# Kernel optimization log

Measured on AMD Instinct MI355X. Metric: run time of the kernel, lower is better.

Reference implementation:

```python
import jax, jax.numpy as jnp
import numpy as np

N, E = 100000, 1600000
IN_DIM, H, D = 128, 4, 32
ALPHA = 0.2  # leaky relu negative slope


def setup_inputs() -> dict:
    key = jax.random.key(0)
    k1, k2, k3, k4, k5, k6 = jax.random.split(key, 6)
    return {
        "inputs": jax.random.normal(k1, (N, IN_DIM), dtype=jnp.float32),
        "src": jax.random.randint(k2, (E,), 0, N, dtype=jnp.int32),
        "dst": jax.random.randint(k3, (E,), 0, N, dtype=jnp.int32),
        "fc_w": jax.random.normal(k4, (IN_DIM, H * D), dtype=jnp.float32) * (1.414 / np.sqrt(IN_DIM)),
        "attn_l": jax.random.normal(k5, (D,), dtype=jnp.float32) * 0.1,
        "attn_r": jax.random.normal(k6, (D,), dtype=jnp.float32) * 0.1,
    }


def reference(inputs, src, dst, fc_w, attn_l, attn_r):
    # fc + reshape to (N, H, D); feat_drop is identity (p=0)
    ft = (inputs @ fc_w).reshape(N, H, D)
    # attn_l/attn_r are (1,1,D) in torch -> broadcast over heads
    a1 = jnp.einsum("nhd,d->nh", ft, attn_l)  # (N, H)
    a2 = jnp.einsum("nhd,d->nh", ft, attn_r)  # (N, H)
    # per-edge logits; original keeps ONLY head-0 scores after edge_softmax
    # (scores[:, 0, :].unsqueeze(1)), so we only need head 0 here.
    e = jax.nn.leaky_relu(a1[src, 0] + a2[dst, 0], ALPHA)  # (E,)
    # numerically-stable segment softmax over destination nodes
    emax = jax.ops.segment_max(e, dst, num_segments=N)
    ex = jnp.exp(e - emax[dst])
    denom = jax.ops.segment_sum(ex, dst, num_segments=N)
    a = ex / denom[dst]  # (E,) broadcast to all heads
    # u_mul_e + sum aggregation; attn_drop is identity (p=0)
    msg = ft[src] * a[:, None, None]  # (E, H, D)
    out = jax.ops.segment_sum(msg, dst, num_segments=N)  # (N, H, D)
    return out
```

## Files before the change

### kernel.cpp

```cpp
#include <hip/hip_runtime.h>


#define ALPHA 0.2f
#define NBLK 512
#define BBITS 8
#define BSIZE 256
#define CAP 5120
#define ESLOTS 1024

typedef __attribute__((ext_vector_type(8))) short bf16x8;
typedef __attribute__((ext_vector_type(8))) unsigned short u16x8;
typedef __attribute__((ext_vector_type(4))) float f32x4;

__device__ __forceinline__ unsigned short f2bf(float f) {
    unsigned u = __float_as_uint(f);
    unsigned r = (u + 0x7FFFu + ((u >> 16) & 1u)) >> 16;
    return (unsigned short)r;
}

__device__ __forceinline__ unsigned mkey(unsigned u) {
    return ((int)u < 0) ? ~u : (u | 0x80000000u);
}
__device__ __forceinline__ float unmkey(unsigned k) {
    unsigned u = ((int)k < 0) ? (k & 0x7FFFFFFFu) : ~k;
    return __uint_as_float(u);
}

__global__ __launch_bounds__(256) void prep_kernel(const float* __restrict__ W,
                                                   u16x8* __restrict__ Wswz) {
    int gt = blockIdx.x * 256 + threadIdx.x;
    if (gt < 2048) {
        int n = gt >> 4, c = gt & 15;
        u16x8 v;
        #pragma unroll
        for (int j = 0; j < 8; ++j) v[j] = f2bf(W[(c * 8 + j) * 128 + n]);
        Wswz[n * 16 + (c ^ (n & 7))] = v;
    }
}

__global__ __launch_bounds__(256) void front_kernel(
        const float* __restrict__ A, const u16x8* __restrict__ Wswz,
        const float* __restrict__ attn_l, const float* __restrict__ attn_r,
        unsigned short* __restrict__ ftb,
        float* __restrict__ s_l, float* __restrict__ s_r, int N, int GB,
        const int* __restrict__ dst, unsigned* __restrict__ bh,
        int E, int nbucket, int slice) {
    __shared__ char smem[49152];
    const int tid = threadIdx.x;

    if (blockIdx.x >= (unsigned)GB) {
        unsigned* cnt = (unsigned*)smem;
        for (int i = tid; i < nbucket; i += 256) cnt[i] = 0u;
        __syncthreads();
        const int b = blockIdx.x - GB;
        int s0 = b * slice, s1 = min(s0 + slice, E);
        for (int i = s0 + tid; i < s1; i += 256)
            atomicAdd(&cnt[((unsigned)dst[i]) >> BBITS], 1u);
        __syncthreads();
        for (int k = tid; k < nbucket; k += 256)
            bh[(size_t)k * NBLK + b] = cnt[k];
        return;
    }

    u16x8* A_lds = (u16x8*)smem;
    u16x8* W_lds = (u16x8*)(smem + 16384);
    const int block_row = blockIdx.x * 64;

    for (int i = tid; i < 2048; i += 256) W_lds[i] = Wswz[i];

    for (int l = tid; l < 1024; l += 256) {
        int m = l >> 4, c = l & 15;
        int row = block_row + m;
        float4 v0 = make_float4(0.f, 0.f, 0.f, 0.f), v1 = v0;
        if (row < N) {
            const float4* p = (const float4*)(A + (size_t)row * 128 + c * 8);
            v0 = p[0]; v1 = p[1];
        }
        u16x8 u;
        u[0] = f2bf(v0.x); u[1] = f2bf(v0.y); u[2] = f2bf(v0.z); u[3] = f2bf(v0.w);
        u[4] = f2bf(v1.x); u[5] = f2bf(v1.y); u[6] = f2bf(v1.z); u[7] = f2bf(v1.w);
        A_lds[m * 16 + (c ^ (m & 7))] = u;
    }
    __syncthreads();

    const int wv = tid >> 6;
    const int lane = tid & 63;
    const int lm = lane & 15;
    const int quad = lane >> 4;

    f32x4 acc[8];
    #pragma unroll
    for (int t = 0; t < 8; ++t) acc[t] = (f32x4)(0.f);

    const int am = wv * 16 + lm;
    #pragma unroll
    for (int ks = 0; ks < 4; ++ks) {
        int c = ks * 4 + quad;
        bf16x8 af = *(const bf16x8*)&A_lds[am * 16 + (c ^ (am & 7))];
        #pragma unroll
        for (int t = 0; t < 8; ++t) {
            int n = t * 16 + lm;
            bf16x8 bf = *(const bf16x8*)&W_lds[n * 16 + (c ^ (n & 7))];
            acc[t] = __builtin_amdgcn_mfma_f32_16x16x32_bf16(af, bf, acc[t], 0, 0, 0);
        }
    }

    {
        float al0 = attn_l[lm], al1 = attn_l[16 + lm];
        float ar0 = attn_r[lm], ar1 = attn_r[16 + lm];
        #pragma unroll
        for (int r = 0; r < 4; ++r) {
            float pl = acc[0][r] * al0 + acc[1][r] * al1;
            float pr = acc[0][r] * ar0 + acc[1][r] * ar1;
            #pragma unroll
            for (int mask = 1; mask < 16; mask <<= 1) {
                pl += __shfl_xor(pl, mask, 64);
                pr += __shfl_xor(pr, mask, 64);
            }
            if (lm == 0) {
                int row = block_row + wv * 16 + quad * 4 + r;
                if (row < N) { s_l[row] = pl; s_r[row] = pr; }
            }
        }
    }

    unsigned short* C_lds = (unsigned short*)A_lds;
    #pragma unroll
    for (int t = 0; t < 8; ++t) {
        #pragma unroll
        for (int r = 0; r < 4; ++r) {
            int mrow = wv * 16 + quad * 4 + r;
            C_lds[mrow * 128 + t * 16 + lm] = f2bf(acc[t][r]);
        }
    }
    __syncthreads();
    for (int l = tid; l < 1024; l += 256) {
        int m = l >> 4, c = l & 15;
        int row = block_row + m;
        if (row < N)
            *(u16x8*)(ftb + (size_t)row * 128 + c * 8) = *(const u16x8*)&C_lds[m * 128 + c * 8];
    }
}

__global__ __launch_bounds__(256) void scan1_kernel(const unsigned* __restrict__ counts,
                                                    unsigned* __restrict__ S,
                                                    unsigned* __restrict__ partials, int M) {
    __shared__ unsigned sh[256];
    const int tid = threadIdx.x;
    const int base = blockIdx.x * 1024 + tid * 4;
    unsigned v[4];
    unsigned s = 0;
    #pragma unroll
    for (int k = 0; k < 4; ++k) {
        int idx = base + k;
        v[k] = (idx < M) ? counts[idx] : 0u;
        s += v[k];
    }
    sh[tid] = s;
    __syncthreads();
    for (int off = 1; off < 256; off <<= 1) {
        unsigned t = (tid >= off) ? sh[tid - off] : 0u;
        __syncthreads();
        sh[tid] += t;
        __syncthreads();
    }
    if (tid == 255) partials[blockIdx.x] = sh[255];
    unsigned run = (tid == 0) ? 0u : sh[tid - 1];
    #pragma unroll
    for (int k = 0; k < 4; ++k) {
        int idx = base + k;
        if (idx < M) S[idx] = run;
        run += v[k];
    }
}

__global__ __launch_bounds__(256) void scan2_kernel(unsigned* __restrict__ partials, int NB) {
    __shared__ unsigned sh[256];
    const int tid = threadIdx.x;
    unsigned v[4];
    unsigned s = 0;
    #pragma unroll
    for (int k = 0; k < 4; ++k) {
        int idx = tid * 4 + k;
        v[k] = (idx < NB) ? partials[idx] : 0u;
        s += v[k];
    }
    sh[tid] = s;
    __syncthreads();
    for (int off = 1; off < 256; off <<= 1) {
        unsigned t = (tid >= off) ? sh[tid - off] : 0u;
        __syncthreads();
        sh[tid] += t;
        __syncthreads();
    }
    unsigned run = (tid == 0) ? 0u : sh[tid - 1];
    #pragma unroll
    for (int k = 0; k < 4; ++k) {
        int idx = tid * 4 + k;
        if (idx < NB) partials[idx] = run;
        run += v[k];
    }
}

__global__ __launch_bounds__(256) void bscatter_kernel(
        const int* __restrict__ src, const int* __restrict__ dst,
        const float* __restrict__ s_l, const float* __restrict__ s_r,
        const unsigned* __restrict__ S, const unsigned* __restrict__ partials,
        uint2* __restrict__ staged, int E, int nbucket, int slice) {
    __shared__ unsigned basel[512];
    __shared__ unsigned cur[512];
    const int b = blockIdx.x;
    for (int k = threadIdx.x; k < nbucket; k += 256) {
        unsigned idx = (unsigned)k * NBLK + b;
        basel[k] = S[idx] + partials[idx >> 10];
        cur[k] = 0u;
    }
    __syncthreads();
    int s0 = b * slice, s1 = min(s0 + slice, E);
    for (int i = s0 + threadIdx.x; i < s1; i += 256) {
        int s = src[i], d = dst[i];
        unsigned k = ((unsigned)d) >> BBITS;
        float x = s_l[s] + s_r[d];
        float e = (x > 0.f) ? x : ALPHA * x;
        unsigned pos = basel[k] + atomicAdd(&cur[k], 1u);
        staged[pos] = make_uint2((unsigned)s | (((unsigned)d & (BSIZE - 1)) << 20),
                                 __float_as_uint(e));
    }
}

__global__ __launch_bounds__(256) void bsort_kernel(
        uint2* __restrict__ staged, const unsigned* __restrict__ S,
        const unsigned* __restrict__ partials,
        unsigned* __restrict__ offsets, int N, int E, int nbucket) {
    __shared__ uint2 rec[CAP];
    __shared__ unsigned cnt[BSIZE], incl[BSIZE], cur[BSIZE], mx[BSIZE];
    __shared__ float sm[BSIZE];
    const int k = blockIdx.x;
    const int t = threadIdx.x;
    unsigned idx0 = (unsigned)k * NBLK;
    unsigned gstart = S[idx0] + partials[idx0 >> 10];
    unsigned gend = (k + 1 == nbucket) ? (unsigned)E
                                       : (S[idx0 + NBLK] + partials[(idx0 + NBLK) >> 10]);
    int n = (int)(gend - gstart);
    if (n > CAP) n = CAP;

    cnt[t] = 0u;
    cur[t] = 0u;
    mx[t] = 0u;
    sm[t] = 0.f;
    __syncthreads();
    for (int i = t; i < n; i += 256) {
        uint2 r = staged[gstart + i];
        rec[i] = r;
        unsigned dl = r.x >> 20;
        atomicAdd(&cnt[dl], 1u);
        atomicMax(&mx[dl], mkey(r.y));
    }
    __syncthreads();
    incl[t] = cnt[t];
    __syncthreads();
    for (int off = 1; off < 256; off <<= 1) {
        unsigned u = (t >= off) ? incl[t - off] : 0u;
        __syncthreads();
        incl[t] += u;
        __syncthreads();
    }
    for (int i = t; i < n; i += 256) {
        uint2 r = rec[i];
        unsigned dl = r.x >> 20;
        atomicAdd(&sm[dl], __expf(__uint_as_float(r.y) - unmkey(mx[dl])));
    }
    __syncthreads();
    float ssum = sm[t];
    sm[t] = (cnt[t] > 0) ? 1.f / ssum : 0.f;
    int d = k * BSIZE + t;
    if (d < N) offsets[d] = gstart + incl[t];
    __syncthreads();
    for (int i = t; i < n; i += 256) {
        uint2 r = rec[i];
        unsigned dl = r.x >> 20;
        float a = __expf(__uint_as_float(r.y) - unmkey(mx[dl])) * sm[dl];
        unsigned p = incl[dl] - cnt[dl] + atomicAdd(&cur[dl], 1u);
        staged[gstart + p] = make_uint2(r.x & 0xFFFFFu, __float_as_uint(a));
    }
}

__global__ __launch_bounds__(256) void aggregate_kernel(
        const uint2* __restrict__ edata, const unsigned* __restrict__ offsets,
        const unsigned short* __restrict__ ftb, float* __restrict__ out, int N) {
    __shared__ uint2 elds[ESLOTS];
    const int wv = threadIdx.x >> 6;
    const int lane = threadIdx.x & 63;
    const int eh = lane >> 4;
    const int j  = lane & 15;
    const int db = blockIdx.x * 4;
    const int d = db + wv;

    const unsigned bstart = (db == 0) ? 0u : offsets[db - 1];
    const unsigned bend = offsets[min(db + 3, N - 1)];
    unsigned start = 0u, end = 0u;
    if (d < N) {
        start = (d == 0) ? 0u : offsets[d - 1];
        end = offsets[d];
    }

    float acc[8] = {0.f, 0.f, 0.f, 0.f, 0.f, 0.f, 0.f, 0.f};

    for (unsigned cbase = bstart; cbase < bend; cbase += ESLOTS) {
        const unsigned cn = min((unsigned)ESLOTS, bend - cbase);
        __syncthreads();
        for (unsigned i = threadIdx.x; i < cn; i += 256)
            elds[i] = edata[cbase + i];
        __syncthreads();
        const unsigned lo = (start > cbase) ? start : cbase;
        const unsigned hi = (end < cbase + cn) ? end : (cbase + cn);
        for (unsigned e = lo; e < hi; e += 16) {
            unsigned i0 = e + eh, i1 = e + 4 + eh, i2 = e + 8 + eh, i3 = e + 12 + eh;
            uint2 e0 = (i0 < hi) ? elds[i0 - cbase] : make_uint2(0u, 0u);
            uint2 e1 = (i1 < hi) ? elds[i1 - cbase] : make_uint2(0u, 0u);
            uint2 e2 = (i2 < hi) ? elds[i2 - cbase] : make_uint2(0u, 0u);
            uint2 e3 = (i3 < hi) ? elds[i3 - cbase] : make_uint2(0u, 0u);
            uint4 q0 = *(const uint4*)(ftb + (size_t)e0.x * 128 + j * 8);
            uint4 q1 = *(const uint4*)(ftb + (size_t)e1.x * 128 + j * 8);
            uint4 q2 = *(const uint4*)(ftb + (size_t)e2.x * 128 + j * 8);
            uint4 q3 = *(const uint4*)(ftb + (size_t)e3.x * 128 + j * 8);
            float a0 = __uint_as_float(e0.y);
            float a1 = __uint_as_float(e1.y);
            float a2 = __uint_as_float(e2.y);
            float a3 = __uint_as_float(e3.y);
            const unsigned* w0 = (const unsigned*)&q0;
            const unsigned* w1 = (const unsigned*)&q1;
            const unsigned* w2 = (const unsigned*)&q2;
            const unsigned* w3 = (const unsigned*)&q3;
            #pragma unroll
            for (int p = 0; p < 4; ++p) {
                acc[2 * p]     += a0 * __uint_as_float(w0[p] << 16);
                acc[2 * p + 1] += a0 * __uint_as_float(w0[p] & 0xFFFF0000u);
                acc[2 * p]     += a1 * __uint_as_float(w1[p] << 16);
                acc[2 * p + 1] += a1 * __uint_as_float(w1[p] & 0xFFFF0000u);
                acc[2 * p]     += a2 * __uint_as_float(w2[p] << 16);
                acc[2 * p + 1] += a2 * __uint_as_float(w2[p] & 0xFFFF0000u);
                acc[2 * p]     += a3 * __uint_as_float(w3[p] << 16);
                acc[2 * p + 1] += a3 * __uint_as_float(w3[p] & 0xFFFF0000u);
            }
        }
    }
    #pragma unroll
    for (int p = 0; p < 8; ++p) {
        acc[p] += __shfl_xor(acc[p], 16, 64);
        acc[p] += __shfl_xor(acc[p], 32, 64);
    }
    if (d < N && eh == 0) {
        float4* op = (float4*)(out + (size_t)d * 128 + j * 8);
        op[0] = make_float4(acc[0], acc[1], acc[2], acc[3]);
        op[1] = make_float4(acc[4], acc[5], acc[6], acc[7]);
    }
}

static inline size_t align256(size_t x) { return (x + 255) & ~(size_t)255; }

extern "C" void kernel_launch(void* const* d_in, const int* in_sizes, int n_in,
                              void* d_out, int out_size, void* d_ws, size_t ws_size,
                              hipStream_t stream) {
    const float* inputs = (const float*)d_in[0];
    const int*   src    = (const int*)d_in[1];
    const int*   dst    = (const int*)d_in[2];
    const float* fc_w   = (const float*)d_in[3];
    const float* attn_l = (const float*)d_in[4];
    const float* attn_r = (const float*)d_in[5];
    float* out = (float*)d_out;

    const int N = in_sizes[0] / 128;
    const int E = in_sizes[1];
    const int nbucket = (N + BSIZE - 1) / BSIZE;
    const int M = nbucket * NBLK;
    const int NB1 = (M + 1023) / 1024;
    const int slice = (E + NBLK - 1) / NBLK;
    const int GB = (N + 63) / 64;

    char* w = (char*)d_ws;
    unsigned short* ftb = (unsigned short*)w;  w += align256((size_t)N * 128 * 2);
    float*    s_l      = (float*)w;     w += align256((size_t)N * 4);
    float*    s_r      = (float*)w;     w += align256((size_t)N * 4);
    unsigned* bh       = (unsigned*)w;  w += align256((size_t)M * 4);
    unsigned* S        = (unsigned*)w;  w += align256((size_t)M * 4);
    unsigned* partials = (unsigned*)w;  w += align256(1024 * 4);
    unsigned* offsets  = (unsigned*)w;  w += align256((size_t)N * 4);
    u16x8*    Wswz     = (u16x8*)w;     w += align256(2048 * 16);
    uint2*    staged   = (uint2*)w;     w += align256((size_t)E * 8);

    prep_kernel<<<8, 256, 0, stream>>>(fc_w, Wswz);
    front_kernel<<<GB + NBLK, 256, 0, stream>>>(inputs, Wswz, attn_l, attn_r,
                                                ftb, s_l, s_r, N, GB,
                                                dst, bh, E, nbucket, slice);
    scan1_kernel<<<NB1, 256, 0, stream>>>(bh, S, partials, M);
    scan2_kernel<<<1, 256, 0, stream>>>(partials, NB1);
    bscatter_kernel<<<NBLK, 256, 0, stream>>>(src, dst, s_l, s_r, S, partials,
                                              staged, E, nbucket, slice);
    bsort_kernel<<<nbucket, 256, 0, stream>>>(staged, S, partials, offsets,
                                              N, E, nbucket);
    aggregate_kernel<<<(N + 3) / 4, 256, 0, stream>>>(staged, offsets, ftb, out, N);
}
```

Measured before the change: 259.0 us.

## Replace bucketed sort with per-node degree counting and fuse softmax into aggregation

Drops the two-level bucket histogram, scatter and in-LDS bucket sort. Node degrees are now counted with global atomics, scanned into exclusive offsets, and each edge is placed directly at its destination slot with a global atomicAdd that doubles as the write cursor. The segment max/sum softmax moves into the aggregate kernel, computed per destination wave from the staged logits. This removes a kernel and a full extra pass over the edge array, at the cost of contended global atomics and unordered edges within each segment.

Result: slower. 344.1 us (+32.9%).

```diff
diff --git a/kernel.cpp b/kernel.cpp
--- a/kernel.cpp
+++ b/kernel.cpp
@@ -2,10 +2,7 @@
 
 
 #define ALPHA 0.2f
-#define NBLK 512
-#define BBITS 8
-#define BSIZE 256
-#define CAP 5120
+#define HB 512
 #define ESLOTS 1024
 
 typedef __attribute__((ext_vector_type(8))) short bf16x8;
@@ -18,16 +15,9 @@
     return (unsigned short)r;
 }
 
-__device__ __forceinline__ unsigned mkey(unsigned u) {
-    return ((int)u < 0) ? ~u : (u | 0x80000000u);
-}
-__device__ __forceinline__ float unmkey(unsigned k) {
-    unsigned u = ((int)k < 0) ? (k & 0x7FFFFFFFu) : ~k;
-    return __uint_as_float(u);
-}
-
 __global__ __launch_bounds__(256) void prep_kernel(const float* __restrict__ W,
-                                                   u16x8* __restrict__ Wswz) {
+                                                   u16x8* __restrict__ Wswz,
+                                                   unsigned* __restrict__ deg, int N) {
     int gt = blockIdx.x * 256 + threadIdx.x;
     if (gt < 2048) {
         int n = gt >> 4, c = gt & 15;
@@ -36,6 +26,7 @@
         for (int j = 0; j < 8; ++j) v[j] = f2bf(W[(c * 8 + j) * 128 + n]);
         Wswz[n * 16 + (c ^ (n & 7))] = v;
     }
+    if (gt < N) deg[gt] = 0u;
 }
 
 __global__ __launch_bounds__(256) void front_kernel(
@@ -43,22 +34,16 @@
         const float* __restrict__ attn_l, const float* __restrict__ attn_r,
         unsigned short* __restrict__ ftb,
         float* __restrict__ s_l, float* __restrict__ s_r, int N, int GB,
-        const int* __restrict__ dst, unsigned* __restrict__ bh,
-        int E, int nbucket, int slice) {
+        const int* __restrict__ dst, unsigned* __restrict__ deg,
+        int E, int slice) {
     __shared__ char smem[49152];
     const int tid = threadIdx.x;
 
     if (blockIdx.x >= (unsigned)GB) {
-        unsigned* cnt = (unsigned*)smem;
-        for (int i = tid; i < nbucket; i += 256) cnt[i] = 0u;
-        __syncthreads();
         const int b = blockIdx.x - GB;
         int s0 = b * slice, s1 = min(s0 + slice, E);
         for (int i = s0 + tid; i < s1; i += 256)
-            atomicAdd(&cnt[((unsigned)dst[i]) >> BBITS], 1u);
-        __syncthreads();
-        for (int k = tid; k < nbucket; k += 256)
-            bh[(size_t)k * NBLK + b] = cnt[k];
+            atomicAdd(&deg[(unsigned)dst[i]], 1u);
         return;
     }
 
@@ -202,91 +187,23 @@
     }
 }
 
-__global__ __launch_bounds__(256) void bscatter_kernel(
+__global__ __launch_bounds__(256) void scatter_kernel(
         const int* __restrict__ src, const int* __restrict__ dst,
         const float* __restrict__ s_l, const float* __restrict__ s_r,
-        const unsigned* __restrict__ S, const unsigned* __restrict__ partials,
-        uint2* __restrict__ staged, int E, int nbucket, int slice) {
-    __shared__ unsigned basel[512];
-    __shared__ unsigned cur[512];
-    const int b = blockIdx.x;
-    for (int k = threadIdx.x; k < nbucket; k += 256) {
-        unsigned idx = (unsigned)k * NBLK + b;
-        basel[k] = S[idx] + partials[idx >> 10];
-        cur[k] = 0u;
-    }
-    __syncthreads();
-    int s0 = b * slice, s1 = min(s0 + slice, E);
-    for (int i = s0 + threadIdx.x; i < s1; i += 256) {
-        int s = src[i], d = dst[i];
-        unsigned k = ((unsigned)d) >> BBITS;
-        float x = s_l[s] + s_r[d];
-        float e = (x > 0.f) ? x : ALPHA * x;
-        unsigned pos = basel[k] + atomicAdd(&cur[k], 1u);
-        staged[pos] = make_uint2((unsigned)s | (((unsigned)d & (BSIZE - 1)) << 20),
-                                 __float_as_uint(e));
-    }
-}
-
-__global__ __launch_bounds__(256) void bsort_kernel(
-        uint2* __restrict__ staged, const unsigned* __restrict__ S,
-        const unsigned* __restrict__ partials,
-        unsigned* __restrict__ offsets, int N, int E, int nbucket) {
-    __shared__ uint2 rec[CAP];
-    __shared__ unsigned cnt[BSIZE], incl[BSIZE], cur[BSIZE], mx[BSIZE];
-    __shared__ float sm[BSIZE];
-    const int k = blockIdx.x;
-    const int t = threadIdx.x;
-    unsigned idx0 = (unsigned)k * NBLK;
-    unsigned gstart = S[idx0] + partials[idx0 >> 10];
-    unsigned gend = (k + 1 == nbucket) ? (unsigned)E
-                                       : (S[idx0 + NBLK] + partials[(idx0 + NBLK) >> 10]);
-    int n = (int)(gend - gstart);
-    if (n > CAP) n = CAP;
-
-    cnt[t] = 0u;
-    cur[t] = 0u;
-    mx[t] = 0u;
-    sm[t] = 0.f;
-    __syncthreads();
-    for (int i = t; i < n; i += 256) {
-        uint2 r = staged[gstart + i];
-        rec[i] = r;
-        unsigned dl = r.x >> 20;
-        atomicAdd(&cnt[dl], 1u);
-        atomicMax(&mx[dl], mkey(r.y));
-    }
-    __syncthreads();
-    incl[t] = cnt[t];
-    __syncthreads();
-    for (int off = 1; off < 256; off <<= 1) {
-        unsigned u = (t >= off) ? incl[t - off] : 0u;
-        __syncthreads();
-        incl[t] += u;
-        __syncthreads();
-    }
-    for (int i = t; i < n; i += 256) {
-        uint2 r = rec[i];
-        unsigned dl = r.x >> 20;
-        atomicAdd(&sm[dl], __expf(__uint_as_float(r.y) - unmkey(mx[dl])));
-    }
-    __syncthreads();
-    float ssum = sm[t];
-    sm[t] = (cnt[t] > 0) ? 1.f / ssum : 0.f;
-    int d = k * BSIZE + t;
-    if (d < N) offsets[d] = gstart + incl[t];
-    __syncthreads();
-    for (int i = t; i < n; i += 256) {
-        uint2 r = rec[i];
-        unsigned dl = r.x >> 20;
-        float a = __expf(__uint_as_float(r.y) - unmkey(mx[dl])) * sm[dl];
-        unsigned p = incl[dl] - cnt[dl] + atomicAdd(&cur[dl], 1u);
-        staged[gstart + p] = make_uint2(r.x & 0xFFFFFu, __float_as_uint(a));
-    }
+        unsigned* __restrict__ S, const unsigned* __restrict__ P,
+        uint2* __restrict__ staged, int E) {
+    int i = blockIdx.x * 256 + threadIdx.x;
+    if (i >= E) return;
+    int s = src[i], d = dst[i];
+    float x = s_l[s] + s_r[d];
+    float e = (x > 0.f) ? x : ALPHA * x;
+    unsigned pos = atomicAdd(&S[d], 1u) + P[((unsigned)d) >> 10];
+    staged[pos] = make_uint2((unsigned)s, __float_as_uint(e));
 }
 
 __global__ __launch_bounds__(256) void aggregate_kernel(
-        const uint2* __restrict__ edata, const unsigned* __restrict__ offsets,
+        const uint2* __restrict__ edata, const unsigned* __restrict__ S,
+        const unsigned* __restrict__ P,
         const unsigned short* __restrict__ ftb, float* __restrict__ out, int N) {
     __shared__ uint2 elds[ESLOTS];
     const int wv = threadIdx.x >> 6;
@@ -296,55 +213,113 @@
     const int db = blockIdx.x * 4;
     const int d = db + wv;
 
-    const unsigned bstart = (db == 0) ? 0u : offsets[db - 1];
-    const unsigned bend = offsets[min(db + 3, N - 1)];
+    const unsigned bstart = (db == 0) ? 0u : (S[db - 1] + P[(unsigned)(db - 1) >> 10]);
+    const int dtop = min(db + 3, N - 1);
+    const unsigned bend = S[dtop] + P[(unsigned)dtop >> 10];
     unsigned start = 0u, end = 0u;
     if (d < N) {
-        start = (d == 0) ? 0u : offsets[d - 1];
-        end = offsets[d];
+        start = (d == 0) ? 0u : (S[d - 1] + P[(unsigned)(d - 1) >> 10]);
+        end = S[d] + P[(unsigned)d >> 10];
     }
 
     float acc[8] = {0.f, 0.f, 0.f, 0.f, 0.f, 0.f, 0.f, 0.f};
 
-    for (unsigned cbase = bstart; cbase < bend; cbase += ESLOTS) {
-        const unsigned cn = min((unsigned)ESLOTS, bend - cbase);
-        __syncthreads();
-        for (unsigned i = threadIdx.x; i < cn; i += 256)
-            elds[i] = edata[cbase + i];
-        __syncthreads();
-        const unsigned lo = (start > cbase) ? start : cbase;
-        const unsigned hi = (end < cbase + cn) ? end : (cbase + cn);
-        for (unsigned e = lo; e < hi; e += 16) {
-            unsigned i0 = e + eh, i1 = e + 4 + eh, i2 = e + 8 + eh, i3 = e + 12 + eh;
-            uint2 e0 = (i0 < hi) ? elds[i0 - cbase] : make_uint2(0u, 0u);
-            uint2 e1 = (i1 < hi) ? elds[i1 - cbase] : make_uint2(0u, 0u);
-            uint2 e2 = (i2 < hi) ? elds[i2 - cbase] : make_uint2(0u, 0u);
-            uint2 e3 = (i3 < hi) ? elds[i3 - cbase] : make_uint2(0u, 0u);
-            uint4 q0 = *(const uint4*)(ftb + (size_t)e0.x * 128 + j * 8);
-            uint4 q1 = *(const uint4*)(ftb + (size_t)e1.x * 128 + j * 8);
-            uint4 q2 = *(const uint4*)(ftb + (size_t)e2.x * 128 + j * 8);
-            uint4 q3 = *(const uint4*)(ftb + (size_t)e3.x * 128 + j * 8);
-            float a0 = __uint_as_float(e0.y);
-            float a1 = __uint_as_float(e1.y);
-            float a2 = __uint_as_float(e2.y);
-            float a3 = __uint_as_float(e3.y);
-            const unsigned* w0 = (const unsigned*)&q0;
-            const unsigned* w1 = (const unsigned*)&q1;
-            const unsigned* w2 = (const unsigned*)&q2;
-            const unsigned* w3 = (const unsigned*)&q3;
-            #pragma unroll
-            for (int p = 0; p < 4; ++p) {
-                acc[2 * p]     += a0 * __uint_as_float(w0[p] << 16);
-                acc[2 * p + 1] += a0 * __uint_as_float(w0[p] & 0xFFFF0000u);
-                acc[2 * p]     += a1 * __uint_as_float(w1[p] << 16);
-                acc[2 * p + 1] += a1 * __uint_as_float(w1[p] & 0xFFFF0000u);
-                acc[2 * p]     += a2 * __uint_as_float(w2[p] << 16);
-                acc[2 * p + 1] += a2 * __uint_as_float(w2[p] & 0xFFFF0000u);
-                acc[2 * p]     += a3 * __uint_as_float(w3[p] << 16);
-                acc[2 * p + 1] += a3 * __uint_as_float(w3[p] & 0xFFFF0000u);
-            }
-        }
-    }
+    if (bend - bstart <= (unsigned)ESLOTS) {
+        for (unsigned i = threadIdx.x; i < bend - bstart; i += 256)
+            elds[i] = edata[bstart + i];
+        __syncthreads();
+        if (d < N && end > start) {
+            float m = -1e30f;
+            for (unsigned i = start + eh; i < end; i += 4)
+                m = fmaxf(m, __uint_as_float(elds[i - bstart].y));
+            m = fmaxf(m, __shfl_xor(m, 16, 64));
+            m = fmaxf(m, __shfl_xor(m, 32, 64));
+            float s = 0.f;
+            for (unsigned i = start + eh; i < end; i += 4) {
+                float w = __expf(__uint_as_float(elds[i - bstart].y) - m);
+                s += w;
+                if (j == 0) elds[i - bstart].y = __float_as_uint(w);
+            }
+            s += __shfl_xor(s, 16, 64);
+            s += __shfl_xor(s, 32, 64);
+            float rden = 1.f / s;
+            for (unsigned e = start; e < end; e += 16) {
+                unsigned i0 = e + eh, i1 = i0 + 4, i2 = i0 + 8, i3 = i0 + 12;
+                uint2 e0 = (i0 < end) ? elds[i0 - bstart] : make_uint2(0u, 0u);
+                uint2 e1 = (i1 < end) ? elds[i1 - bstart] : make_uint2(0u, 0u);
+                uint2 e2 = (i2 < end) ? elds[i2 - bstart] : make_uint2(0u, 0u);
+                uint2 e3 = (i3 < end) ? elds[i3 - bstart] : make_uint2(0u, 0u);
+                uint4 q0 = *(const uint4*)(ftb + (size_t)e0.x * 128 + j * 8);
+                uint4 q1 = *(const uint4*)(ftb + (size_t)e1.x * 128 + j * 8);
+                uint4 q2 = *(const uint4*)(ftb + (size_t)e2.x * 128 + j * 8);
+                uint4 q3 = *(const uint4*)(ftb + (size_t)e3.x * 128 + j * 8);
+                float a0 = __uint_as_float(e0.y) * rden;
+                float a1 = __uint_as_float(e1.y) * rden;
+                float a2 = __uint_as_float(e2.y) * rden;
+                float a3 = __uint_as_float(e3.y) * rden;
+                const unsigned* w0 = (const unsigned*)&q0;
+                const unsigned* w1 = (const unsigned*)&q1;
+                const unsigned* w2 = (const unsigned*)&q2;
+                const unsigned* w3 = (const unsigned*)&q3;
+                #pragma unroll
+                for (int p = 0; p < 4; ++p) {
+                    acc[2 * p]     += a0 * __uint_as_float(w0[p] << 16);
+                    acc[2 * p + 1] += a0 * __uint_as_float(w0[p] & 0xFFFF0000u);
+                    acc[2 * p]     += a1 * __uint_as_float(w1[p] << 16);
+                    acc[2 * p + 1] += a1 * __uint_as_float(w1[p] & 0xFFFF0000u);
+                    acc[2 * p]     += a2 * __uint_as_float(w2[p] << 16);
+                    acc[2 * p + 1] += a2 * __uint_as_float(w2[p] & 0xFFFF0000u);
+                    acc[2 * p]     += a3 * __uint_as_float(w3[p] << 16);
+                    acc[2 * p + 1] += a3 * __uint_as_float(w3[p] & 0xFFFF0000u);
+                }
+            }
+        }
+    } else {
+        if (d < N && end > start) {
+            float m = -1e30f;
+            for (unsigned i = start + eh; i < end; i += 4)
+                m = fmaxf(m, __uint_as_float(edata[i].y));
+            m = fmaxf(m, __shfl_xor(m, 16, 64));
+            m = fmaxf(m, __shfl_xor(m, 32, 64));
+            float s = 0.f;
+            for (unsigned i = start + eh; i < end; i += 4)
+                s += __expf(__uint_as_float(edata[i].y) - m);
+            s += __shfl_xor(s, 16, 64);
+            s += __shfl_xor(s, 32, 64);
+            float rden = 1.f / s;
+            for (unsigned e = start; e < end; e += 16) {
+                unsigned i0 = e + eh, i1 = i0 + 4, i2 = i0 + 8, i3 = i0 + 12;
+                uint2 e0 = (i0 < end) ? edata[i0] : make_uint2(0u, 0u);
+                uint2 e1 = (i1 < end) ? edata[i1] : make_uint2(0u, 0u);
+                uint2 e2 = (i2 < end) ? edata[i2] : make_uint2(0u, 0u);
+                uint2 e3 = (i3 < end) ? edata[i3] : make_uint2(0u, 0u);
+                uint4 q0 = *(const uint4*)(ftb + (size_t)e0.x * 128 + j * 8);
+                uint4 q1 = *(const uint4*)(ftb + (size_t)e1.x * 128 + j * 8);
+                uint4 q2 = *(const uint4*)(ftb + (size_t)e2.x * 128 + j * 8);
+                uint4 q3 = *(const uint4*)(ftb + (size_t)e3.x * 128 + j * 8);
+                float a0 = (i0 < end) ? __expf(__uint_as_float(e0.y) - m) * rden : 0.f;
+                float a1 = (i1 < end) ? __expf(__uint_as_float(e1.y) - m) * rden : 0.f;
+                float a2 = (i2 < end) ? __expf(__uint_as_float(e2.y) - m) * rden : 0.f;
+                float a3 = (i3 < end) ? __expf(__uint_as_float(e3.y) - m) * rden : 0.f;
+                const unsigned* w0 = (const unsigned*)&q0;
+                const unsigned* w1 = (const unsigned*)&q1;
+                const unsigned* w2 = (const unsigned*)&q2;
+                const unsigned* w3 = (const unsigned*)&q3;
+                #pragma unroll
+                for (int p = 0; p < 4; ++p) {
+                    acc[2 * p]     += a0 * __uint_as_float(w0[p] << 16);
+                    acc[2 * p + 1] += a0 * __uint_as_float(w0[p] & 0xFFFF0000u);
+                    acc[2 * p]     += a1 * __uint_as_float(w1[p] << 16);
+                    acc[2 * p + 1] += a1 * __uint_as_float(w1[p] & 0xFFFF0000u);
+                    acc[2 * p]     += a2 * __uint_as_float(w2[p] << 16);
+                    acc[2 * p + 1] += a2 * __uint_as_float(w2[p] & 0xFFFF0000u);
+                    acc[2 * p]     += a3 * __uint_as_float(w3[p] << 16);
+                    acc[2 * p + 1] += a3 * __uint_as_float(w3[p] & 0xFFFF0000u);
+                }
+            }
+        }
+    }
+
     #pragma unroll
     for (int p = 0; p < 8; ++p) {
         acc[p] += __shfl_xor(acc[p], 16, 64);
@@ -372,32 +347,28 @@
 
     const int N = in_sizes[0] / 128;
     const int E = in_sizes[1];
-    const int nbucket = (N + BSIZE - 1) / BSIZE;
-    const int M = nbucket * NBLK;
-    const int NB1 = (M + 1023) / 1024;
-    const int slice = (E + NBLK - 1) / NBLK;
+    const int NB1 = (N + 1023) / 1024;
+    const int slice = (E + HB - 1) / HB;
     const int GB = (N + 63) / 64;
 
     char* w = (char*)d_ws;
     unsigned short* ftb = (unsigned short*)w;  w += align256((size_t)N * 128 * 2);
     float*    s_l      = (float*)w;     w += align256((size_t)N * 4);
     float*    s_r      = (float*)w;     w += align256((size_t)N * 4);
-    unsigned* bh       = (unsigned*)w;  w += align256((size_t)M * 4);
-    unsigned* S        = (unsigned*)w;  w += align256((size_t)M * 4);
+    unsigned* deg      = (unsigned*)w;  w += align256((size_t)N * 4);
+    unsigned* S        = (unsigned*)w;  w += align256((size_t)N * 4);
     unsigned* partials = (unsigned*)w;  w += align256(1024 * 4);
-    unsigned* offsets  = (unsigned*)w;  w += align256((size_t)N * 4);
     u16x8*    Wswz     = (u16x8*)w;     w += align256(2048 * 16);
     uint2*    staged   = (uint2*)w;     w += align256((size_t)E * 8);
 
-    prep_kernel<<<8, 256, 0, stream>>>(fc_w, Wswz);
-    front_kernel<<<GB + NBLK, 256, 0, stream>>>(inputs, Wswz, attn_l, attn_r,
-                                                ftb, s_l, s_r, N, GB,
-                                                dst, bh, E, nbucket, slice);
-    scan1_kernel<<<NB1, 256, 0, stream>>>(bh, S, partials, M);
+    prep_kernel<<<(N + 255) / 256, 256, 0, stream>>>(fc_w, Wswz, deg, N);
+    front_kernel<<<GB + HB, 256, 0, stream>>>(inputs, Wswz, attn_l, attn_r,
+                                              ftb, s_l, s_r, N, GB,
+                                              dst, deg, E, slice);
+    scan1_kernel<<<NB1, 256, 0, stream>>>(deg, S, partials, N);
     scan2_kernel<<<1, 256, 0, stream>>>(partials, NB1);
-    bscatter_kernel<<<NBLK, 256, 0, stream>>>(src, dst, s_l, s_r, S, partials,
-                                              staged, E, nbucket, slice);
-    bsort_kernel<<<nbucket, 256, 0, stream>>>(staged, S, partials, offsets,
-                                              N, E, nbucket);
-    aggregate_kernel<<<(N + 3) / 4, 256, 0, stream>>>(staged, offsets, ftb, out, N);
-}
+    scatter_kernel<<<(E + 255) / 256, 256, 0, stream>>>(src, dst, s_l, s_r,
+                                                        S, partials, staged, E);
+    aggregate_kernel<<<(N + 3) / 4, 256, 0, stream>>>(staged, S, partials,
+                                                      ftb, out, N);
+}
```

## Load GEMM A fragments directly to registers and restructure bucket softmax per-thread

Applied to the files above, without the earlier changes.

The front GEMM kernel now reads input rows straight from global memory into per-lane bf16 fragments instead of staging them through LDS, which shrinks shared memory to 32KB and should allow more blocks per CU. The bucket-sort kernel is reorganised: it counts and scans first, scatters records into LDS already sorted by destination, then has one thread per destination compute max, sum and normalisation serially over its contiguous segment. This removes the LDS atomicMax, the atomic float adds and the separate exp passes, at the cost of reading staged data twice from global memory and doing serial per-thread loops that are unbalanced for high-degree nodes. The A-fragment loads are uncoalesced per lane (strided row reads), which may hurt the GEMM's memory efficiency.

New measurement: 246.8 us. -4.7%, faster.

```diff
diff --git a/kernel.cpp b/kernel.cpp
--- a/kernel.cpp
+++ b/kernel.cpp
@@ -16,14 +16,6 @@
     unsigned u = __float_as_uint(f);
     unsigned r = (u + 0x7FFFu + ((u >> 16) & 1u)) >> 16;
     return (unsigned short)r;
-}
-
-__device__ __forceinline__ unsigned mkey(unsigned u) {
-    return ((int)u < 0) ? ~u : (u | 0x80000000u);
-}
-__device__ __forceinline__ float unmkey(unsigned k) {
-    unsigned u = ((int)k < 0) ? (k & 0x7FFFFFFFu) : ~k;
-    return __uint_as_float(u);
 }
 
 __global__ __launch_bounds__(256) void prep_kernel(const float* __restrict__ W,
@@ -45,7 +37,7 @@
         float* __restrict__ s_l, float* __restrict__ s_r, int N, int GB,
         const int* __restrict__ dst, unsigned* __restrict__ bh,
         int E, int nbucket, int slice) {
-    __shared__ char smem[49152];
+    __shared__ char smem[32768];
     const int tid = threadIdx.x;
 
     if (blockIdx.x >= (unsigned)GB) {
@@ -62,46 +54,46 @@
         return;
     }
 
-    u16x8* A_lds = (u16x8*)smem;
-    u16x8* W_lds = (u16x8*)(smem + 16384);
+    u16x8* W_lds = (u16x8*)smem;
     const int block_row = blockIdx.x * 64;
 
     for (int i = tid; i < 2048; i += 256) W_lds[i] = Wswz[i];
-
-    for (int l = tid; l < 1024; l += 256) {
-        int m = l >> 4, c = l & 15;
-        int row = block_row + m;
-        float4 v0 = make_float4(0.f, 0.f, 0.f, 0.f), v1 = v0;
-        if (row < N) {
-            const float4* p = (const float4*)(A + (size_t)row * 128 + c * 8);
-            v0 = p[0]; v1 = p[1];
-        }
-        u16x8 u;
-        u[0] = f2bf(v0.x); u[1] = f2bf(v0.y); u[2] = f2bf(v0.z); u[3] = f2bf(v0.w);
-        u[4] = f2bf(v1.x); u[5] = f2bf(v1.y); u[6] = f2bf(v1.z); u[7] = f2bf(v1.w);
-        A_lds[m * 16 + (c ^ (m & 7))] = u;
-    }
-    __syncthreads();
 
     const int wv = tid >> 6;
     const int lane = tid & 63;
     const int lm = lane & 15;
     const int quad = lane >> 4;
-
-    f32x4 acc[8];
-    #pragma unroll
-    for (int t = 0; t < 8; ++t) acc[t] = (f32x4)(0.f);
-
-    const int am = wv * 16 + lm;
+    const int am = block_row + wv * 16 + lm;
+    const bool rowok = (am < N);
+
+    bf16x8 a_frag[4];
     #pragma unroll
     for (int ks = 0; ks < 4; ++ks) {
         int c = ks * 4 + quad;
-        bf16x8 af = *(const bf16x8*)&A_lds[am * 16 + (c ^ (am & 7))];
+        float4 v0 = make_float4(0.f, 0.f, 0.f, 0.f), v1 = v0;
+        if (rowok) {
+            const float4* p = (const float4*)(A + (size_t)am * 128 + c * 8);
+            v0 = p[0]; v1 = p[1];
+        }
+        u16x8 u;
+        u[0] = f2bf(v0.x); u[1] = f2bf(v0.y); u[2] = f2bf(v0.z); u[3] = f2bf(v0.w);
+        u[4] = f2bf(v1.x); u[5] = f2bf(v1.y); u[6] = f2bf(v1.z); u[7] = f2bf(v1.w);
+        a_frag[ks] = *(const bf16x8*)&u;
+    }
+    __syncthreads();
+
+    f32x4 acc[8];
+    #pragma unroll
+    for (int t = 0; t < 8; ++t) acc[t] = (f32x4)(0.f);
+
+    #pragma unroll
+    for (int ks = 0; ks < 4; ++ks) {
+        int c = ks * 4 + quad;
         #pragma unroll
         for (int t = 0; t < 8; ++t) {
             int n = t * 16 + lm;
             bf16x8 bf = *(const bf16x8*)&W_lds[n * 16 + (c ^ (n & 7))];
-            acc[t] = __builtin_amdgcn_mfma_f32_16x16x32_bf16(af, bf, acc[t], 0, 0, 0);
+            acc[t] = __builtin_amdgcn_mfma_f32_16x16x32_bf16(a_frag[ks], bf, acc[t], 0, 0, 0);
         }
     }
 
@@ -124,7 +116,8 @@
         }
     }
 
-    unsigned short* C_lds = (unsigned short*)A_lds;
+    __syncthreads();
+    unsigned short* C_lds = (unsigned short*)smem;
     #pragma unroll
     for (int t = 0; t < 8; ++t) {
         #pragma unroll
@@ -233,8 +226,7 @@
         const unsigned* __restrict__ partials,
         unsigned* __restrict__ offsets, int N, int E, int nbucket) {
     __shared__ uint2 rec[CAP];
-    __shared__ unsigned cnt[BSIZE], incl[BSIZE], cur[BSIZE], mx[BSIZE];
-    __shared__ float sm[BSIZE];
+    __shared__ unsigned cnt[BSIZE], incl[BSIZE], cur[BSIZE];
     const int k = blockIdx.x;
     const int t = threadIdx.x;
     unsigned idx0 = (unsigned)k * NBLK;
@@ -245,43 +237,46 @@
     if (n > CAP) n = CAP;
 
     cnt[t] = 0u;
+    __syncthreads();
+    for (int i = t; i < n; i += 256)
+        atomicAdd(&cnt[staged[gstart + i].x >> 20], 1u);
+    __syncthreads();
+    incl[t] = cnt[t];
+    __syncthreads();
+    for (int off = 1; off < 256; off <<= 1) {
+        unsigned u = (t >= off) ? incl[t - off] : 0u;
+        __syncthreads();
+        incl[t] += u;
+        __syncthreads();
+    }
     cur[t] = 0u;
-    mx[t] = 0u;
-    sm[t] = 0.f;
     __syncthreads();
     for (int i = t; i < n; i += 256) {
         uint2 r = staged[gstart + i];
-        rec[i] = r;
         unsigned dl = r.x >> 20;
-        atomicAdd(&cnt[dl], 1u);
-        atomicMax(&mx[dl], mkey(r.y));
-    }
-    __syncthreads();
-    incl[t] = cnt[t];
-    __syncthreads();
-    for (int off = 1; off < 256; off <<= 1) {
-        unsigned u = (t >= off) ? incl[t - off] : 0u;
-        __syncthreads();
-        incl[t] += u;
-        __syncthreads();
-    }
+        unsigned p = incl[dl] - cnt[dl] + atomicAdd(&cur[dl], 1u);
+        rec[p] = r;
+    }
+    __syncthreads();
+    int d = k * BSIZE + t;
+    if (d < N) {
+        int b0 = (int)(incl[t] - cnt[t]);
+        int c = (int)cnt[t];
+        float m = -1e30f;
+        for (int j = 0; j < c; ++j) m = fmaxf(m, __uint_as_float(rec[b0 + j].y));
+        float sum = 0.f;
+        for (int j = 0; j < c; ++j) sum += __expf(__uint_as_float(rec[b0 + j].y) - m);
+        float rden = (c > 0) ? 1.f / sum : 0.f;
+        for (int j = 0; j < c; ++j) {
+            float a = __expf(__uint_as_float(rec[b0 + j].y) - m) * rden;
+            rec[b0 + j].y = __float_as_uint(a);
+        }
+        offsets[d] = gstart + incl[t];
+    }
+    __syncthreads();
     for (int i = t; i < n; i += 256) {
         uint2 r = rec[i];
-        unsigned dl = r.x >> 20;
-        atomicAdd(&sm[dl], __expf(__uint_as_float(r.y) - unmkey(mx[dl])));
-    }
-    __syncthreads();
-    float ssum = sm[t];
-    sm[t] = (cnt[t] > 0) ? 1.f / ssum : 0.f;
-    int d = k * BSIZE + t;
-    if (d < N) offsets[d] = gstart + incl[t];
-    __syncthreads();
-    for (int i = t; i < n; i += 256) {
-        uint2 r = rec[i];
-        unsigned dl = r.x >> 20;
-        float a = __expf(__uint_as_float(r.y) - unmkey(mx[dl])) * sm[dl];
-        unsigned p = incl[dl] - cnt[dl] + atomicAdd(&cur[dl], 1u);
-        staged[gstart + p] = make_uint2(r.x & 0xFFFFFu, __float_as_uint(a));
+        staged[gstart + i] = make_uint2(r.x & 0xFFFFFu, r.y);
     }
 }
 
```
